# Kernel optimization log

Measured on AMD Instinct MI355X. Metric: run time of the kernel, lower is better.

Reference implementation:

```python
import jax, jax.numpy as jnp
import numpy as np

E, P, K, V, H, NE = 768, 256, 32, 32, 128, 8
B, M_DIM, T_DIM = 16, 4, 512


def setup_inputs() -> dict:
    key = jax.random.key(0)
    ks = jax.random.split(key, 24)
    s = 0.05
    inp = {
        'token_embeddings': jax.random.normal(ks[0], (B, M_DIM, T_DIM, E), jnp.float32),
        'U': jax.random.uniform(ks[1], (B, M_DIM, T_DIM), jnp.float32),
        'R': jax.random.uniform(ks[2], (B, M_DIM, M_DIM, T_DIM), jnp.float32),
        'S': jax.random.uniform(ks[3], (B, M_DIM, M_DIM, T_DIM), jnp.float32),
        'W_tp': jax.random.normal(ks[4], (E, P), jnp.float32) * s,
        'b_tp': jnp.zeros((P,), jnp.float32),
        'W_q': jax.random.normal(ks[5], (P, K), jnp.float32) * s,
        'b_q': jnp.zeros((K,), jnp.float32),
        'W_k': jax.random.normal(ks[6], (2, K), jnp.float32) * s,
        'b_k': jnp.zeros((K,), jnp.float32),
        'W_v': jax.random.normal(ks[7], (2, V), jnp.float32) * s,
        'b_v': jnp.zeros((V,), jnp.float32),
        'W_ih': jax.random.normal(ks[8], (3 * H, 1 + V), jnp.float32) * s,
        'W_hh': jax.random.normal(ks[9], (3 * H, H), jnp.float32) * s,
        'b_ih': jnp.zeros((3 * H,), jnp.float32),
        'b_hh': jnp.zeros((3 * H,), jnp.float32),
        'W1': jax.random.normal(ks[10], (P + H, (P + H) // 2), jnp.float32) * s,
        'b1': jnp.zeros(((P + H) // 2,), jnp.float32),
        'W2': jax.random.normal(ks[11], ((P + H) // 2, NE), jnp.float32) * s,
        'b2': jnp.zeros((NE,), jnp.float32),
        'M': M_DIM,
        'T': T_DIM,
    }
    return inp


def _gru(x, W_ih, W_hh, b_ih, b_hh):
    # x: [N, T, D] -> outputs [N, T, H]; PyTorch GRU cell math
    N, T, _ = x.shape
    Hh = W_hh.shape[1]
    gi = jnp.einsum('ntd,gd->ntg', x, W_ih) + b_ih  # [N,T,3H] precomputed input gates
    gi = jnp.transpose(gi, (1, 0, 2))  # [T,N,3H]

    def step(h, gi_t):
        gh = h @ W_hh.T + b_hh
        i_r, i_z, i_n = jnp.split(gi_t, 3, axis=-1)
        h_r, h_z, h_n = jnp.split(gh, 3, axis=-1)
        r = jax.nn.sigmoid(i_r + h_r)
        z = jax.nn.sigmoid(i_z + h_z)
        n = jnp.tanh(i_n + r * h_n)
        h_new = (1.0 - z) * n + z * h
        return h_new, h_new

    h0 = jnp.zeros((N, Hh), x.dtype)
    _, hs = jax.lax.scan(step, h0, gi)
    return jnp.transpose(hs, (1, 0, 2))  # [N,T,H]


def reference(token_embeddings, U, R, S, W_tp, b_tp, W_q, b_q, W_k, b_k, W_v, b_v,
              W_ih, W_hh, b_ih, b_hh, W1, b1, W2, b2, M, T):
    Bn, Mn, Tn, _ = token_embeddings.shape
    proc = jax.nn.relu(token_embeddings @ W_tp + b_tp)           # [B,M,T,P]
    query = proc @ W_q + b_q                                     # [B,M,T,K]
    Rp = jnp.transpose(R, (0, 3, 1, 2))                          # [B,T,M,M]
    Sp = jnp.transpose(S, (0, 3, 1, 2))
    pf = jnp.stack([Rp, Sp], axis=-1)                            # [B,T,M,M,2]
    keys = pf @ W_k + b_k                                        # [B,T,M,M,K]
    vals = pf @ W_v + b_v                                        # [B,T,M,M,V]
    scores = jnp.einsum('bmtk,btmjk->bmtj', query, keys) / np.sqrt(K)
    diag = jnp.eye(Mn, dtype=bool)                               # exclude j == m
    scores = jnp.where(diag[None, :, None, :], -1e9, scores)
    w = jax.nn.softmax(scores, axis=-1)                          # [B,M,T,M]
    ctx = jnp.einsum('bmtj,btmjv->bmtv', w, vals)                # [B,M,T,V]
    gru_in = jnp.concatenate([U[..., None], ctx], axis=-1)       # [B,M,T,1+V]
    gru_out = _gru(gru_in.reshape(Bn * Mn, Tn, 1 + V), W_ih, W_hh, b_ih, b_hh)
    rus_ctx = gru_out.reshape(Bn, Mn, Tn, H)
    combined = jnp.concatenate([proc, rus_ctx], axis=-1)         # [B,M,T,P+H]
    hidden = jax.nn.relu(combined @ W1 + b1)
    logits = hidden @ W2 + b2                                    # [B,M,T,NE]
    return logits
```

## Files before the change

### kernel.cpp

```cpp
#include <hip/hip_runtime.h>


typedef __attribute__((ext_vector_type(8))) short short8;
typedef __attribute__((ext_vector_type(4))) float f32x4;

__device__ __forceinline__ float bf2f(unsigned short u) {
    return __uint_as_float(((unsigned int)u) << 16);
}
__device__ __forceinline__ unsigned short f2bf(float f) {
    unsigned int x = __float_as_uint(f);
    return (unsigned short)((x + 0x7FFFu + ((x >> 16) & 1u)) >> 16);
}
__device__ __forceinline__ float sigm(float x) { return 1.0f / (1.0f + __expf(-x)); }
__device__ __forceinline__ float tanh_fast(float x) {
    x = fminf(fmaxf(x, -15.0f), 15.0f);
    float e = __expf(-2.0f * x);
    return (1.0f - e) / (1.0f + e);
}
__device__ __forceinline__ float dpp_xor1_add(float v) {
    int o = __builtin_amdgcn_update_dpp(0, __float_as_int(v), 0xB1, 0xF, 0xF, true);
    return v + __int_as_float(o);
}
__device__ __forceinline__ float sel4(f32x4 c, int sel) {
    float t0 = (sel & 1) ? c[1] : c[0];
    float t1 = (sel & 1) ? c[3] : c[2];
    return (sel & 2) ? t1 : t0;
}

#define CST_SC   768
#define CST_WU   800
#define CST_WA2  1184
#define CST_WB2  1568
#define CST_CC   1952

__global__ void k_paint(float* out, float val, int nmax) {
    int i = blockIdx.x * blockDim.x + threadIdx.x;
    if (i < nmax) out[i] = val;
}

__global__ void k_prep(const float* __restrict__ Wq,
                       const float* __restrict__ bq,
                       const float* __restrict__ Wk,
                       const float* __restrict__ bk,
                       const float* __restrict__ Wv,
                       const float* __restrict__ bv,
                       const float* __restrict__ Wih,
                       const float* __restrict__ bih,
                       float* __restrict__ cst)
{
    const int t = threadIdx.x;
    if (t < 256) {
        float a = 0.f, b = 0.f, c = 0.f;
        for (int k = 0; k < 32; ++k) {
            float w = Wq[t * 32 + k];
            a = fmaf(w, Wk[k], a);
            b = fmaf(w, Wk[32 + k], b);
            c = fmaf(w, bk[k], c);
        }
        cst[t] = a; cst[256 + t] = b; cst[512 + t] = c;
    }
    if (t == 0) {
        float ca = 0.f, cb = 0.f, cc = 0.f;
        for (int k = 0; k < 32; ++k) {
            float bqk = bq[k];
            ca = fmaf(bqk, Wk[k], ca);
            cb = fmaf(bqk, Wk[32 + k], cb);
            cc = fmaf(bqk, bk[k], cc);
        }
        cst[CST_SC + 0] = ca; cst[CST_SC + 1] = cb; cst[CST_SC + 2] = cc;
    }
    if (t < 384) {
        cst[CST_WU + t] = Wih[t * 33];
        float a2 = 0.f, b2 = 0.f, c2 = bih[t];
        for (int v = 0; v < 32; ++v) {
            float w = Wih[t * 33 + 1 + v];
            a2 = fmaf(w, Wv[v], a2);
            b2 = fmaf(w, Wv[32 + v], b2);
            c2 = fmaf(w, bv[v], c2);
        }
        cst[CST_WA2 + t] = a2; cst[CST_WB2 + t] = b2; cst[CST_CC + t] = c2;
    }
}

__global__ __launch_bounds__(256) void k_proc(
    const float* __restrict__ A,
    const float* __restrict__ Bw,
    const float* __restrict__ bias,
    unsigned short* __restrict__ C)
{
    __shared__ unsigned short A_s[128 * 40];
    __shared__ unsigned short B_s[64 * 40];
    const int t = threadIdx.x;
    const int row0 = blockIdx.y * 128;
    const int col0 = blockIdx.x * 64;
    const int lane = t & 63, wave = t >> 6;
    const int wr = wave >> 1, wc = wave & 1;
    const int quad = lane >> 4, l16 = lane & 15;

    f32x4 acc[4][2] = {};

    for (int k0 = 0; k0 < 768; k0 += 32) {
        {
            const int r = t >> 1, kq = (t & 1) * 16;
            const float* src = A + (size_t)(row0 + r) * 768 + k0 + kq;
            float4 v0 = *(const float4*)(src);
            float4 v1 = *(const float4*)(src + 4);
            float4 v2 = *(const float4*)(src + 8);
            float4 v3 = *(const float4*)(src + 12);
            short8 s0, s1;
            s0[0] = f2bf(v0.x); s0[1] = f2bf(v0.y); s0[2] = f2bf(v0.z); s0[3] = f2bf(v0.w);
            s0[4] = f2bf(v1.x); s0[5] = f2bf(v1.y); s0[6] = f2bf(v1.z); s0[7] = f2bf(v1.w);
            s1[0] = f2bf(v2.x); s1[1] = f2bf(v2.y); s1[2] = f2bf(v2.z); s1[3] = f2bf(v2.w);
            s1[4] = f2bf(v3.x); s1[5] = f2bf(v3.y); s1[6] = f2bf(v3.z); s1[7] = f2bf(v3.w);
            *(short8*)(A_s + r * 40 + kq) = s0;
            *(short8*)(A_s + r * 40 + kq + 8) = s1;
        }
        {
            const int k = t >> 3, nq = (t & 7) * 8;
            const float* src = Bw + (size_t)(k0 + k) * 256 + col0 + nq;
            float4 v0 = *(const float4*)(src);
            float4 v1 = *(const float4*)(src + 4);
            B_s[(nq + 0) * 40 + k] = f2bf(v0.x);
            B_s[(nq + 1) * 40 + k] = f2bf(v0.y);
            B_s[(nq + 2) * 40 + k] = f2bf(v0.z);
            B_s[(nq + 3) * 40 + k] = f2bf(v0.w);
            B_s[(nq + 4) * 40 + k] = f2bf(v1.x);
            B_s[(nq + 5) * 40 + k] = f2bf(v1.y);
            B_s[(nq + 6) * 40 + k] = f2bf(v1.z);
            B_s[(nq + 7) * 40 + k] = f2bf(v1.w);
        }
        __syncthreads();
        short8 af[4], bf[2];
        #pragma unroll
        for (int im = 0; im < 4; ++im)
            af[im] = *(const short8*)(A_s + (wr * 64 + im * 16 + l16) * 40 + quad * 8);
        #pragma unroll
        for (int in = 0; in < 2; ++in)
            bf[in] = *(const short8*)(B_s + (wc * 32 + in * 16 + l16) * 40 + quad * 8);
        #pragma unroll
        for (int im = 0; im < 4; ++im)
            #pragma unroll
            for (int in = 0; in < 2; ++in)
                acc[im][in] = __builtin_amdgcn_mfma_f32_16x16x32_bf16(
                    af[im], bf[in], acc[im][in], 0, 0, 0);
        __syncthreads();
    }
    float bias_v[2];
    #pragma unroll
    for (int in = 0; in < 2; ++in) bias_v[in] = bias[col0 + wc * 32 + in * 16 + l16];
    #pragma unroll
    for (int im = 0; im < 4; ++im)
        #pragma unroll
        for (int in = 0; in < 2; ++in) {
            const int c_g = col0 + wc * 32 + in * 16 + l16;
            #pragma unroll
            for (int reg = 0; reg < 4; ++reg) {
                const int r_g = row0 + wr * 64 + im * 16 + quad * 4 + reg;
                float v = fmaxf(acc[im][in][reg] + bias_v[in], 0.f);
                C[(size_t)r_g * 256 + c_g] = f2bf(v);
            }
        }
}

__global__ __launch_bounds__(256) void k_gru(
    const unsigned short* __restrict__ proc,
    const float* __restrict__ U,
    const float* __restrict__ Rg,
    const float* __restrict__ Sg,
    const float* __restrict__ Whh,
    const float* __restrict__ bhh,
    const float* __restrict__ cst,
    unsigned short* __restrict__ gout)
{
    __shared__ unsigned short hbuf[2][2][144];
    __shared__ float4 uvw_s[512];
    __shared__ float wv_s[768];

    const int tid  = threadIdx.x;
    const int lane = tid & 63, w = tid >> 6;
    const int l16  = lane & 15, quad = lane >> 4;
    const int n    = blockIdx.x;
    const int par  = l16 & 1;
    const int sel  = (l16 >> 1) & 3;
    const int hh   = (l16 >> 3) & 1;
    const int eg   = 32 * w + 16 * hh + quad * 4 + sel;
    const bool writer = (par == 0);

    short8 afr[3][2][4];
    #pragma unroll
    for (int g3 = 0; g3 < 3; ++g3)
        #pragma unroll
        for (int h2 = 0; h2 < 2; ++h2) {
            const int row = g3 * 128 + 32 * w + 16 * h2 + l16;
            const float* rp = Whh + (size_t)row * 128 + quad * 8;
            #pragma unroll
            for (int kf = 0; kf < 4; ++kf) {
                float4 v0 = *(const float4*)(rp + kf * 32);
                float4 v1 = *(const float4*)(rp + kf * 32 + 4);
                short8 s;
                s[0] = f2bf(v0.x); s[1] = f2bf(v0.y); s[2] = f2bf(v0.z); s[3] = f2bf(v0.w);
                s[4] = f2bf(v1.x); s[5] = f2bf(v1.y); s[6] = f2bf(v1.z); s[7] = f2bf(v1.w);
                afr[g3][h2][kf] = s;
            }
        }

    const float wu_r = cst[CST_WU  + eg], wu_z = cst[CST_WU  + 128 + eg], wu_n = cst[CST_WU  + 256 + eg];
    const float wa_r = cst[CST_WA2 + eg], wa_z = cst[CST_WA2 + 128 + eg], wa_n = cst[CST_WA2 + 256 + eg];
    const float wb_r = cst[CST_WB2 + eg], wb_z = cst[CST_WB2 + 128 + eg], wb_n = cst[CST_WB2 + 256 + eg];
    const float cc_r = cst[CST_CC  + eg] + bhh[eg];
    const float cc_z = cst[CST_CC  + 128 + eg] + bhh[128 + eg];
    const float cc_n = cst[CST_CC  + 256 + eg];
    const float bh_n = bhh[256 + eg];

    for (int i = tid; i < 768; i += 256) wv_s[i] = cst[i];
    for (int i = tid; i < 288; i += 256) ((unsigned int*)hbuf)[i] = 0u;
    __syncthreads();

    {
        const float scA = cst[CST_SC + 0], scB = cst[CST_SC + 1], scC = cst[CST_SC + 2];
        const int m = n & 3;
        const float scale = 0.17677669529663687f;
        for (int rr = tid; rr < 512; rr += 256) {
            const unsigned short* pr = proc + ((size_t)n * 512 + rr) * 256;
            float dA = scA, dB = scB, dC = scC;
            for (int kk = 0; kk < 256; kk += 8) {
                short8 v = *(const short8*)(pr + kk);
                #pragma unroll
                for (int e = 0; e < 8; ++e) {
                    const float f = bf2f((unsigned short)v[e]);
                    dA = fmaf(f, wv_s[kk + e], dA);
                    dB = fmaf(f, wv_s[256 + kk + e], dB);
                    dC = fmaf(f, wv_s[512 + kk + e], dC);
                }
            }
            float rv[4], sv[4], sc4[4], mx = -1e30f;
            #pragma unroll
            for (int j = 0; j < 4; ++j) {
                const size_t idx = ((size_t)(4 * n + j)) * 512 + rr;
                rv[j] = Rg[idx]; sv[j] = Sg[idx];
                float v = (rv[j] * dA + sv[j] * dB + dC) * scale;
                if (j == m) v = -1e9f;
                sc4[j] = v; mx = fmaxf(mx, v);
            }
            float wj[4], se = 0.f;
            #pragma unroll
            for (int j = 0; j < 4; ++j) { wj[j] = __expf(sc4[j] - mx); se += wj[j]; }
            const float inv = 1.0f / se;
            float wrk = 0.f, wsk = 0.f;
            #pragma unroll
            for (int j = 0; j < 4; ++j) { wrk += wj[j] * rv[j]; wsk += wj[j] * sv[j]; }
            float4 p;
            p.x = U[(size_t)n * 512 + rr];
            p.y = wrk * inv; p.z = wsk * inv; p.w = 0.f;
            uvw_s[rr] = p;
        }
    }
    __syncthreads();

    float h_old = 0.f;
    const f32x4 ZZ = {0.f, 0.f, 0.f, 0.f};

    #pragma unroll 2
    for (int t = 0; t < 512; ++t) {
        const int cur = t & 1, nxt = cur ^ 1;

        const unsigned short* hb = &hbuf[cur][par][0];
        short8 bfr[4];
        #pragma unroll
        for (int kf = 0; kf < 4; ++kf)
            bfr[kf] = *(const short8*)(hb + kf * 32 + quad * 8);
        const float4 uvw = uvw_s[t];

        f32x4 c[6] = {ZZ, ZZ, ZZ, ZZ, ZZ, ZZ};
        #pragma unroll
        for (int kf = 0; kf < 4; ++kf)
            #pragma unroll
            for (int j = 0; j < 6; ++j)
                c[j] = __builtin_amdgcn_mfma_f32_16x16x32_bf16(
                    afr[j >> 1][j & 1][kf], bfr[kf], c[j], 0, 0, 0);

        float gh[3];
        #pragma unroll
        for (int g3 = 0; g3 < 3; ++g3) {
            const float v0 = sel4(c[2 * g3 + 0], sel);
            const float v1 = sel4(c[2 * g3 + 1], sel);
            gh[g3] = dpp_xor1_add(hh ? v1 : v0);
        }

        const float gir = fmaf(uvw.z, wb_r, fmaf(uvw.y, wa_r, fmaf(uvw.x, wu_r, cc_r)));
        const float giz = fmaf(uvw.z, wb_z, fmaf(uvw.y, wa_z, fmaf(uvw.x, wu_z, cc_z)));
        const float gin = fmaf(uvw.z, wb_n, fmaf(uvw.y, wa_n, fmaf(uvw.x, wu_n, cc_n)));
        const float r  = sigm(gir + gh[0]);
        const float z  = sigm(giz + gh[1]);
        const float nn = tanh_fast(fmaf(r, gh[2] + bh_n, gin));
        const float hn = fmaf(z, h_old - nn, nn);
        h_old = hn;

        if (writer) {
            const unsigned short hi16 = f2bf(hn);
            hbuf[nxt][0][eg] = hi16;
            hbuf[nxt][1][eg] = f2bf(hn - bf2f(hi16));
            gout[((size_t)n * 512 + t) * 128 + eg] = hi16;
        }
        asm volatile("s_waitcnt lgkmcnt(0)" ::: "memory");
        __builtin_amdgcn_s_barrier();
        asm volatile("" ::: "memory");
        __builtin_amdgcn_sched_barrier(0x7);
    }
}

__global__ __launch_bounds__(256) void k_hid(
    const unsigned short* __restrict__ proc,
    const unsigned short* __restrict__ gout,
    const float* __restrict__ W1,
    const float* __restrict__ b1,
    const float* __restrict__ W2,
    const float* __restrict__ b2,
    float* __restrict__ out)
{
    __shared__ __align__(16) unsigned char smem[56480];
    unsigned short* As = (unsigned short*)smem;
    unsigned short* Bh = (unsigned short*)(smem + 5120);
    unsigned short* Bl = (unsigned short*)(smem + 20480);
    float* Hs  = (float*)smem;
    float* W2t = (float*)(smem + 50176);
    float* b2s = (float*)(smem + 56448);

    const int tid = threadIdx.x;
    const int row0 = blockIdx.x * 64;
    const int lane = tid & 63, w = tid >> 6;
    const int l16 = lane & 15, quad = lane >> 4;

    for (int i = tid; i < 1536; i += 256) {
        const int c = i >> 3, e = i & 7;
        W2t[e * 196 + c] = W2[i];
    }
    if (tid < 8) b2s[tid] = b2[tid];

    const int ar = tid >> 2, akq = (tid & 3) * 8;
    const int bk2 = (tid >> 4) * 2, bc0 = tid & 15;

    f32x4 acc[4][3] = {};

    for (int k0 = 0; k0 < 384; k0 += 32) {
        __syncthreads();
        {
            const int kk = k0 + akq;
            short8 v;
            if (kk < 256) v = *(const short8*)(proc + (size_t)(row0 + ar) * 256 + kk);
            else          v = *(const short8*)(gout + (size_t)(row0 + ar) * 128 + (kk - 256));
            *(short8*)(As + ar * 40 + akq) = v;
        }
        {
            const float* wrow0 = W1 + (size_t)(k0 + bk2) * 192;
            const float* wrow1 = wrow0 + 192;
            #pragma unroll
            for (int j = 0; j < 12; ++j) {
                const int c = bc0 + 16 * j;
                const float f0 = wrow0[c], f1 = wrow1[c];
                const unsigned short h0 = f2bf(f0), h1 = f2bf(f1);
                const unsigned short s0 = f2bf(f0 - bf2f(h0));
                const unsigned short s1 = f2bf(f1 - bf2f(h1));
                *(unsigned int*)(Bh + c * 40 + bk2) = (unsigned int)h0 | ((unsigned int)h1 << 16);
                *(unsigned int*)(Bl + c * 40 + bk2) = (unsigned int)s0 | ((unsigned int)s1 << 16);
            }
        }
        __syncthreads();
        short8 af[4], bh[3], bl[3];
        #pragma unroll
        for (int m = 0; m < 4; ++m)
            af[m] = *(const short8*)(As + (m * 16 + l16) * 40 + quad * 8);
        #pragma unroll
        for (int nn = 0; nn < 3; ++nn) {
            const int col = w * 48 + nn * 16 + l16;
            bh[nn] = *(const short8*)(Bh + col * 40 + quad * 8);
            bl[nn] = *(const short8*)(Bl + col * 40 + quad * 8);
        }
        #pragma unroll
        for (int m = 0; m < 4; ++m)
            #pragma unroll
            for (int nn = 0; nn < 3; ++nn) {
                acc[m][nn] = __builtin_amdgcn_mfma_f32_16x16x32_bf16(af[m], bh[nn], acc[m][nn], 0, 0, 0);
                acc[m][nn] = __builtin_amdgcn_mfma_f32_16x16x32_bf16(af[m], bl[nn], acc[m][nn], 0, 0, 0);
            }
    }
    __syncthreads();
    {
        float b1v[3];
        #pragma unroll
        for (int nn = 0; nn < 3; ++nn) b1v[nn] = b1[w * 48 + nn * 16 + l16];
        #pragma unroll
        for (int m = 0; m < 4; ++m)
            #pragma unroll
            for (int nn = 0; nn < 3; ++nn) {
                const int col = w * 48 + nn * 16 + l16;
                #pragma unroll
                for (int reg = 0; reg < 4; ++reg) {
                    const int row = m * 16 + quad * 4 + reg;
                    Hs[row * 196 + col] = fmaxf(acc[m][nn][reg] + b1v[nn], 0.f);
                }
            }
    }
    __syncthreads();
    const int r = tid >> 2, qq = tid & 3;
    const int e0 = 2 * qq, e1 = e0 + 1;
    float s0 = b2s[e0], s1 = b2s[e1];
    const float* hrow = Hs + r * 196;
    const float* w0 = W2t + e0 * 196;
    const float* w1 = W2t + e1 * 196;
    #pragma unroll 8
    for (int c = 0; c < 192; c += 4) {
        float4 h4 = *(const float4*)(hrow + c);
        float4 a4 = *(const float4*)(w0 + c);
        float4 b4 = *(const float4*)(w1 + c);
        s0 = fmaf(h4.x, a4.x, fmaf(h4.y, a4.y, fmaf(h4.z, a4.z, fmaf(h4.w, a4.w, s0))));
        s1 = fmaf(h4.x, b4.x, fmaf(h4.y, b4.y, fmaf(h4.z, b4.z, fmaf(h4.w, b4.w, s1))));
    }
    out[(size_t)(row0 + r) * 8 + e0] = s0;
    out[(size_t)(row0 + r) * 8 + e1] = s1;
}

extern "C" void kernel_launch(void* const* d_in, const int* in_sizes, int n_in,
                              void* d_out, int out_size, void* d_ws, size_t ws_size,
                              hipStream_t stream) {
    const float* emb  = (const float*)d_in[0];
    const float* U    = (const float*)d_in[1];
    const float* R    = (const float*)d_in[2];
    const float* S    = (const float*)d_in[3];
    const float* W_tp = (const float*)d_in[4];
    const float* b_tp = (const float*)d_in[5];
    const float* W_q  = (const float*)d_in[6];
    const float* b_q  = (const float*)d_in[7];
    const float* W_k  = (const float*)d_in[8];
    const float* b_k  = (const float*)d_in[9];
    const float* W_v  = (const float*)d_in[10];
    const float* b_v  = (const float*)d_in[11];
    const float* W_ih = (const float*)d_in[12];
    const float* W_hh = (const float*)d_in[13];
    const float* b_ih = (const float*)d_in[14];
    const float* b_hh = (const float*)d_in[15];
    const float* W1   = (const float*)d_in[16];
    const float* b1   = (const float*)d_in[17];
    const float* W2   = (const float*)d_in[18];
    const float* b2   = (const float*)d_in[19];

    float* outp = (float*)d_out;

    const size_t NEEDED = 25444352u;
    if (ws_size < NEEDED) {
        k_paint<<<(out_size + 255) / 256, 256, 0, stream>>>(outp, 3.0f, out_size);
        return;
    }

    char* ws = (char*)d_ws;
    unsigned short* proc = (unsigned short*)(ws);
    unsigned short* gout = (unsigned short*)(ws + 17039360u);
    float*          cst  = (float*)(ws + 25427968u);

    k_prep<<<1, 512, 0, stream>>>(W_q, b_q, W_k, b_k, W_v, b_v, W_ih, b_ih, cst);
    k_proc<<<dim3(4, 256), 256, 0, stream>>>(emb, W_tp, b_tp, proc);
    k_gru <<<64, 256, 0, stream>>>(proc, U, R, S, W_hh, b_hh, cst, gout);
    k_hid <<<512, 256, 0, stream>>>(proc, gout, W1, b1, W2, b2, outp);
}
```

Measured before the change: 530.2 us.

## Fuse attention score dot-products into projection GEMM epilogue via atomics

The three per-row dot products of proc against the folded query-key weights move out of the GRU kernel's serial preamble and into the k_proc epilogue. Each wave reduces partial sums across lanes with shuffles and accumulates them into a zeroed partial buffer with atomics. k_gru then reads three floats per row instead of scanning 256 bf16 values, which shortens the low-parallelism 64-block GRU launch. The cost is extra shuffles and atomics in the GEMM epilogue, plus a zeroing pass in k_prep, which now runs on more blocks.

```diff
diff --git a/kernel.cpp b/kernel.cpp
--- a/kernel.cpp
+++ b/kernel.cpp
@@ -46,46 +46,53 @@
                        const float* __restrict__ bv,
                        const float* __restrict__ Wih,
                        const float* __restrict__ bih,
-                       float* __restrict__ cst)
+                       float* __restrict__ cst,
+                       float* __restrict__ part)
 {
     const int t = threadIdx.x;
-    if (t < 256) {
-        float a = 0.f, b = 0.f, c = 0.f;
-        for (int k = 0; k < 32; ++k) {
-            float w = Wq[t * 32 + k];
-            a = fmaf(w, Wk[k], a);
-            b = fmaf(w, Wk[32 + k], b);
-            c = fmaf(w, bk[k], c);
-        }
-        cst[t] = a; cst[256 + t] = b; cst[512 + t] = c;
-    }
-    if (t == 0) {
-        float ca = 0.f, cb = 0.f, cc = 0.f;
-        for (int k = 0; k < 32; ++k) {
-            float bqk = bq[k];
-            ca = fmaf(bqk, Wk[k], ca);
-            cb = fmaf(bqk, Wk[32 + k], cb);
-            cc = fmaf(bqk, bk[k], cc);
-        }
-        cst[CST_SC + 0] = ca; cst[CST_SC + 1] = cb; cst[CST_SC + 2] = cc;
-    }
-    if (t < 384) {
-        cst[CST_WU + t] = Wih[t * 33];
-        float a2 = 0.f, b2 = 0.f, c2 = bih[t];
-        for (int v = 0; v < 32; ++v) {
-            float w = Wih[t * 33 + 1 + v];
-            a2 = fmaf(w, Wv[v], a2);
-            b2 = fmaf(w, Wv[32 + v], b2);
-            c2 = fmaf(w, bv[v], c2);
-        }
-        cst[CST_WA2 + t] = a2; cst[CST_WB2 + t] = b2; cst[CST_CC + t] = c2;
-    }
+    if (blockIdx.x == 0) {
+        if (t < 256) {
+            float a = 0.f, b = 0.f, c = 0.f;
+            for (int k = 0; k < 32; ++k) {
+                float w = Wq[t * 32 + k];
+                a = fmaf(w, Wk[k], a);
+                b = fmaf(w, Wk[32 + k], b);
+                c = fmaf(w, bk[k], c);
+            }
+            cst[t] = a; cst[256 + t] = b; cst[512 + t] = c;
+        }
+        if (t == 0) {
+            float ca = 0.f, cb = 0.f, cc = 0.f;
+            for (int k = 0; k < 32; ++k) {
+                float bqk = bq[k];
+                ca = fmaf(bqk, Wk[k], ca);
+                cb = fmaf(bqk, Wk[32 + k], cb);
+                cc = fmaf(bqk, bk[k], cc);
+            }
+            cst[CST_SC + 0] = ca; cst[CST_SC + 1] = cb; cst[CST_SC + 2] = cc;
+        }
+        if (t < 384) {
+            cst[CST_WU + t] = Wih[t * 33];
+            float a2 = 0.f, b2 = 0.f, c2 = bih[t];
+            for (int v = 0; v < 32; ++v) {
+                float w = Wih[t * 33 + 1 + v];
+                a2 = fmaf(w, Wv[v], a2);
+                b2 = fmaf(w, Wv[32 + v], b2);
+                c2 = fmaf(w, bv[v], c2);
+            }
+            cst[CST_WA2 + t] = a2; cst[CST_WB2 + t] = b2; cst[CST_CC + t] = c2;
+        }
+    }
+    const int gt = blockIdx.x * 512 + t;
+    for (int i = gt; i < 131072; i += 4096) part[i] = 0.f;
 }
 
 __global__ __launch_bounds__(256) void k_proc(
     const float* __restrict__ A,
     const float* __restrict__ Bw,
     const float* __restrict__ bias,
+    const float* __restrict__ cst,
+    float* __restrict__ part,
     unsigned short* __restrict__ C)
 {
     __shared__ unsigned short A_s[128 * 40];
@@ -145,25 +152,45 @@
                     af[im], bf[in], acc[im][in], 0, 0, 0);
         __syncthreads();
     }
-    float bias_v[2];
+    float bias_v[2], wAv[2], wBv[2], wCv[2];
     #pragma unroll
-    for (int in = 0; in < 2; ++in) bias_v[in] = bias[col0 + wc * 32 + in * 16 + l16];
+    for (int in = 0; in < 2; ++in) {
+        const int c_g = col0 + wc * 32 + in * 16 + l16;
+        bias_v[in] = bias[c_g];
+        wAv[in] = cst[c_g]; wBv[in] = cst[256 + c_g]; wCv[in] = cst[512 + c_g];
+    }
     #pragma unroll
     for (int im = 0; im < 4; ++im)
         #pragma unroll
-        for (int in = 0; in < 2; ++in) {
-            const int c_g = col0 + wc * 32 + in * 16 + l16;
-            #pragma unroll
-            for (int reg = 0; reg < 4; ++reg) {
-                const int r_g = row0 + wr * 64 + im * 16 + quad * 4 + reg;
+        for (int reg = 0; reg < 4; ++reg) {
+            const int r_g = row0 + wr * 64 + im * 16 + quad * 4 + reg;
+            float vA = 0.f, vB = 0.f, vC = 0.f;
+            #pragma unroll
+            for (int in = 0; in < 2; ++in) {
+                const int c_g = col0 + wc * 32 + in * 16 + l16;
                 float v = fmaxf(acc[im][in][reg] + bias_v[in], 0.f);
                 C[(size_t)r_g * 256 + c_g] = f2bf(v);
+                vA = fmaf(v, wAv[in], vA);
+                vB = fmaf(v, wBv[in], vB);
+                vC = fmaf(v, wCv[in], vC);
+            }
+            #pragma unroll
+            for (int mk = 1; mk < 16; mk <<= 1) {
+                vA += __shfl_xor(vA, mk, 64);
+                vB += __shfl_xor(vB, mk, 64);
+                vC += __shfl_xor(vC, mk, 64);
+            }
+            if (l16 == 0) {
+                float* pp = part + (size_t)r_g * 4;
+                atomicAdd(pp + 0, vA);
+                atomicAdd(pp + 1, vB);
+                atomicAdd(pp + 2, vC);
             }
         }
 }
 
 __global__ __launch_bounds__(256) void k_gru(
-    const unsigned short* __restrict__ proc,
+    const float* __restrict__ part,
     const float* __restrict__ U,
     const float* __restrict__ Rg,
     const float* __restrict__ Sg,
@@ -174,7 +201,6 @@
 {
     __shared__ unsigned short hbuf[2][2][144];
     __shared__ float4 uvw_s[512];
-    __shared__ float wv_s[768];
 
     const int tid  = threadIdx.x;
     const int lane = tid & 63, w = tid >> 6;
@@ -212,27 +238,15 @@
     const float cc_n = cst[CST_CC  + 256 + eg];
     const float bh_n = bhh[256 + eg];
 
-    for (int i = tid; i < 768; i += 256) wv_s[i] = cst[i];
     for (int i = tid; i < 288; i += 256) ((unsigned int*)hbuf)[i] = 0u;
-    __syncthreads();
 
     {
         const float scA = cst[CST_SC + 0], scB = cst[CST_SC + 1], scC = cst[CST_SC + 2];
         const int m = n & 3;
         const float scale = 0.17677669529663687f;
         for (int rr = tid; rr < 512; rr += 256) {
-            const unsigned short* pr = proc + ((size_t)n * 512 + rr) * 256;
-            float dA = scA, dB = scB, dC = scC;
-            for (int kk = 0; kk < 256; kk += 8) {
-                short8 v = *(const short8*)(pr + kk);
-                #pragma unroll
-                for (int e = 0; e < 8; ++e) {
-                    const float f = bf2f((unsigned short)v[e]);
-                    dA = fmaf(f, wv_s[kk + e], dA);
-                    dB = fmaf(f, wv_s[256 + kk + e], dB);
-                    dC = fmaf(f, wv_s[512 + kk + e], dC);
-                }
-            }
+            float4 pd = *(const float4*)(part + (size_t)(n * 512 + rr) * 4);
+            const float dA = scA + pd.x, dB = scB + pd.y, dC = scC + pd.z;
             float rv[4], sv[4], sc4[4], mx = -1e30f;
             #pragma unroll
             for (int j = 0; j < 4; ++j) {
@@ -446,7 +460,7 @@
 
     float* outp = (float*)d_out;
 
-    const size_t NEEDED = 25444352u;
+    const size_t NEEDED = 25961600u;
     if (ws_size < NEEDED) {
         k_paint<<<(out_size + 255) / 256, 256, 0, stream>>>(outp, 3.0f, out_size);
         return;
@@ -456,9 +470,10 @@
     unsigned short* proc = (unsigned short*)(ws);
     unsigned short* gout = (unsigned short*)(ws + 17039360u);
     float*          cst  = (float*)(ws + 25427968u);
-
-    k_prep<<<1, 512, 0, stream>>>(W_q, b_q, W_k, b_k, W_v, b_v, W_ih, b_ih, cst);
-    k_proc<<<dim3(4, 256), 256, 0, stream>>>(emb, W_tp, b_tp, proc);
-    k_gru <<<64, 256, 0, stream>>>(proc, U, R, S, W_hh, b_hh, cst, gout);
+    float*          part = (float*)(ws + 25437312u);
+
+    k_prep<<<8, 512, 0, stream>>>(W_q, b_q, W_k, b_k, W_v, b_v, W_ih, b_ih, cst, part);
+    k_proc<<<dim3(4, 256), 256, 0, stream>>>(emb, W_tp, b_tp, cst, part, proc);
+    k_gru <<<64, 256, 0, stream>>>(part, U, R, S, W_hh, b_hh, cst, gout);
     k_hid <<<512, 256, 0, stream>>>(proc, gout, W1, b1, W2, b2, outp);
 }
```

Result: slower. 543.4 us (+2.5%).
